# Performance work log

Hardware: AMD Instinct MI355X
Metric: run time of the kernel (lower is better)

Reference implementation:

```python
import jax, jax.numpy as jnp
import numpy as np
from math import factorial

# (mul, l, parity) for in1 == in2 == out
IRREPS = [(32, 0, 1), (32, 1, -1), (32, 2, 1)]
FEAT_DIM = sum(m * (2 * l + 1) for m, l, _ in IRREPS)  # 288
BATCH = 8192


def _cg(j1, m1, j2, m2, j3, m3):
    # Clebsch-Gordan <j1 m1 j2 m2 | j3 m3> (Racah formula), complex SH basis
    if m1 + m2 != m3 or not (abs(j1 - j2) <= j3 <= j1 + j2):
        return 0.0
    f = factorial
    pre = (2 * j3 + 1) * f(j3 + j1 - j2) * f(j3 - j1 + j2) * f(j1 + j2 - j3) / f(j1 + j2 + j3 + 1)
    pre *= f(j3 + m3) * f(j3 - m3) * f(j1 - m1) * f(j1 + m1) * f(j2 - m2) * f(j2 + m2)
    s = 0.0
    for k in range(0, j1 + j2 - j3 + 1):
        a = [k, j1 + j2 - j3 - k, j1 - m1 - k, j2 + m2 - k, j3 - j2 + m1 + k, j3 - j1 - m2 + k]
        if min(a) < 0:
            continue
        s += (-1.0) ** k / (f(a[0]) * f(a[1]) * f(a[2]) * f(a[3]) * f(a[4]) * f(a[5]))
    return np.sqrt(pre) * s


def _q(l):
    # unitary change of basis: real SH coords = Q @ complex SH coords
    Q = np.zeros((2 * l + 1, 2 * l + 1), dtype=np.complex128)
    Q[l, l] = 1.0
    for m in range(1, l + 1):
        Q[l + m, l + m] = (-1.0) ** m / np.sqrt(2.0)
        Q[l + m, l - m] = 1.0 / np.sqrt(2.0)
        Q[l - m, l - m] = 1j / np.sqrt(2.0)
        Q[l - m, l + m] = -1j * (-1.0) ** m / np.sqrt(2.0)
    return Q


def _wigner3j(l1, l2, l3):
    # real-basis Wigner 3j tensor, unit Frobenius norm (e3nn convention up to sign)
    C = np.zeros((2 * l1 + 1, 2 * l2 + 1, 2 * l3 + 1), dtype=np.complex128)
    for m1 in range(-l1, l1 + 1):
        for m2 in range(-l2, l2 + 1):
            m3 = -(m1 + m2)
            if abs(m3) <= l3:
                C[m1 + l1, m2 + l2, m3 + l3] = (-1.0) ** (l1 - l2 - m3) * _cg(l1, m1, l2, m2, l3, -m3)
    T = np.einsum('mnp,am,bn,cp->abc', C, _q(l1).conj(), _q(l2).conj(), _q(l3).conj())
    T = T.real if np.abs(T.real).sum() >= np.abs(T.imag).sum() else T.imag
    return (T / np.linalg.norm(T)).astype(np.float32)


def _instructions():
    # all parity- and triangle-allowed fully-connected 'uvw' paths
    ins = []
    for i1, (m1, l1, p1) in enumerate(IRREPS):
        for i2, (m2, l2, p2) in enumerate(IRREPS):
            for io, (mo, lo, po) in enumerate(IRREPS):
                if p1 * p2 == po and abs(l1 - l2) <= lo <= l1 + l2:
                    ins.append((i1, i2, io))
    return ins


N_WEIGHT = sum(IRREPS[i1][0] * IRREPS[i2][0] * IRREPS[io][0] for i1, i2, io in _instructions())  # 360448


def setup_inputs() -> dict:
    key = jax.random.key(0)
    k1, k2, k3 = jax.random.split(key, 3)
    return {
        'x1': jax.random.normal(k1, (BATCH, FEAT_DIM), jnp.float32),
        'x2': jax.random.normal(k2, (BATCH, FEAT_DIM), jnp.float32),
        'weight': jax.random.normal(k3, (N_WEIGHT,), jnp.float32),
    }


def _tp(x1, x2, weight):
    ins = _instructions()
    fan = {}
    for i1, i2, io in ins:  # 'element' path normalization fan-in per output irrep
        fan[io] = fan.get(io, 0) + IRREPS[i1][0] * IRREPS[i2][0]
    offs, o = [], 0
    for m, l, _ in IRREPS:
        offs.append(o)
        o += m * (2 * l + 1)
    z = x1.shape[0]
    out = [jnp.zeros((z, m * (2 * l + 1)), x1.dtype) for m, l, _ in IRREPS]
    w_off = 0
    for i1, i2, io in ins:
        m1, l1, _ = IRREPS[i1]
        m2, l2, _ = IRREPS[i2]
        mo, lo, _ = IRREPS[io]
        x1p = x1[:, offs[i1]:offs[i1] + m1 * (2 * l1 + 1)].reshape(z, m1, 2 * l1 + 1)
        x2p = x2[:, offs[i2]:offs[i2] + m2 * (2 * l2 + 1)].reshape(z, m2, 2 * l2 + 1)
        nw = m1 * m2 * mo
        W = weight[w_off:w_off + nw].reshape(m1, m2, mo)
        w_off += nw
        w3 = jnp.asarray(_wigner3j(l1, l2, lo))
        alpha = float(np.sqrt((2 * lo + 1) / fan[io]))  # component norm * 1/sqrt(fan_in)
        # contraction order chosen to keep intermediates small:
        t = jnp.einsum('zui,uvw->zivw', x1p, W)             # [z, 2l1+1, m2, mo]
        y = jnp.einsum('zivw,zvj,ijk->zwk', t, x2p, w3, optimize='optimal')
        out[io] = out[io] + alpha * y.reshape(z, -1)
    return jnp.concatenate(out, axis=1)


def reference(x1, x2, weight):
    return _tp(x1, x2, weight)
```

## Files before the change

### kernel.cpp

```cpp
#include <hip/hip_runtime.h>


__device__ float g_w3[11 * 128];


__device__ __forceinline__ double dfact(int n) {
    double r = 1.0;
    for (int i = 2; i <= n; ++i) r *= (double)i;
    return r;
}

__device__ double cg_coef(int j1, int m1, int j2, int m2, int j3, int m3) {
    if (m1 + m2 != m3) return 0.0;
    int lo = (j1 > j2) ? (j1 - j2) : (j2 - j1);
    if (j3 > j1 + j2 || j3 < lo) return 0.0;
    double pre = (2.0 * j3 + 1.0) * dfact(j3 + j1 - j2) * dfact(j3 - j1 + j2) *
                 dfact(j1 + j2 - j3) / dfact(j1 + j2 + j3 + 1);
    pre *= dfact(j3 + m3) * dfact(j3 - m3) * dfact(j1 - m1) * dfact(j1 + m1) *
           dfact(j2 - m2) * dfact(j2 + m2);
    double s = 0.0;
    for (int k = 0; k <= j1 + j2 - j3; ++k) {
        int a1 = j1 + j2 - j3 - k, a2 = j1 - m1 - k, a3 = j2 + m2 - k;
        int a4 = j3 - j2 + m1 + k, a5 = j3 - j1 - m2 + k;
        if (a1 < 0 || a2 < 0 || a3 < 0 || a4 < 0 || a5 < 0) continue;
        double t = 1.0 / (dfact(k) * dfact(a1) * dfact(a2) * dfact(a3) * dfact(a4) * dfact(a5));
        s += (k & 1) ? -t : t;
    }
    return sqrt(pre) * s;
}

__device__ __forceinline__ void qval(int l, int a, int mi, double& re, double& im) {
    re = 0.0; im = 0.0;
    const double inv = 0.7071067811865475244;
    int ma = a - l, mc = mi - l;
    if (ma == 0) { if (mc == 0) re = 1.0; return; }
    if (ma > 0) {
        if (mc == ma)        re = (ma & 1) ? -inv : inv;
        else if (mc == -ma)  re = inv;
    } else {
        int mm = -ma;
        if (mc == ma)        im = inv;
        else if (mc == -ma)  im = -((mm & 1) ? -inv : inv);
    }
}

__global__ void wigner3j_setup() {
    const int L1[11] = {0,0,0,1,1,1,1,2,2,2,2};
    const int L2[11] = {0,1,2,0,1,1,2,0,1,2,2};
    const int L3[11] = {0,1,2,1,0,2,1,2,1,0,2};
    const int p = blockIdx.x;
    const int l1 = L1[p], l2 = L2[p], l3 = L3[p];
    const int d1 = 2 * l1 + 1, d2 = 2 * l2 + 1, d3 = 2 * l3 + 1;
    const int n = d1 * d2 * d3;

    __shared__ double sre[125], sim[125];
    __shared__ double s_scale;
    __shared__ int s_im;

    const int e = threadIdx.x;
    if (e < n) {
        int a = e / (d2 * d3);
        int r = e - a * d2 * d3;
        int b = r / d3;
        int c = r - b * d3;
        double tre = 0.0, tim = 0.0;
        for (int m1 = -l1; m1 <= l1; ++m1) {
            for (int m2 = -l2; m2 <= l2; ++m2) {
                int m3 = -(m1 + m2);
                if (m3 < -l3 || m3 > l3) continue;
                int ex = l1 - l2 - m3;
                double sgn = (ex % 2 != 0) ? -1.0 : 1.0;
                double C = sgn * cg_coef(l1, m1, l2, m2, l3, -m3);
                if (C == 0.0) continue;
                double r1, i1, r2, i2, r3, i3;
                qval(l1, a, m1 + l1, r1, i1);
                qval(l2, b, m2 + l2, r2, i2);
                qval(l3, c, m3 + l3, r3, i3);
                i1 = -i1; i2 = -i2; i3 = -i3;
                double rr = r1 * r2 - i1 * i2;
                double ri = r1 * i2 + i1 * r2;
                double fr = rr * r3 - ri * i3;
                double fi = rr * i3 + ri * r3;
                tre += C * fr;
                tim += C * fi;
            }
        }
        sre[e] = tre; sim[e] = tim;
    }
    __syncthreads();
    if (threadIdx.x == 0) {
        double sar = 0.0, sai = 0.0;
        for (int i = 0; i < n; ++i) { sar += fabs(sre[i]); sai += fabs(sim[i]); }
        int useim = (sar >= sai) ? 0 : 1;
        double ss = 0.0;
        for (int i = 0; i < n; ++i) { double v = useim ? sim[i] : sre[i]; ss += v * v; }
        s_scale = 1.0 / sqrt(ss);
        s_im = useim;
    }
    __syncthreads();
    if (e < n) {
        double v = s_im ? sim[e] : sre[e];
        g_w3[p * 128 + e] = (float)(v * s_scale);
    }
}


__device__ __forceinline__ float f4c(const float4& v, int c) {
    switch (c & 3) {
        case 0:  return v.x;
        case 1:  return v.y;
        case 2:  return v.z;
        default: return v.w;
    }
}

template <int DH, int DS, int D1, int D2, int DO, bool HX1, int NW>
__device__ __forceinline__ void do_path(const float* __restrict__ xh,
                                        const float* __restrict__ xs,
                                        const float* __restrict__ Wp,
                                        const float* __restrict__ w3p,
                                        int k, float* __restrict__ acc) {
    float w3l[DH][DS];
#pragma unroll
    for (int ih = 0; ih < DH; ++ih) {
#pragma unroll
        for (int is = 0; is < DS; ++is) {
            const int i = HX1 ? ih : is;
            const int j = HX1 ? is : ih;
            w3l[ih][is] = w3p[(i * D2 + j) * DO + k];
        }
    }
    constexpr int CH = (DH >= 5) ? 16 : 32;
    static_assert((CH * DH) % 4 == 0, "H chunk must be float4-tileable");
#pragma unroll 1
    for (int h0 = 0; h0 < 32; h0 += CH) {
        float H[CH * DH];
#pragma unroll
        for (int q = 0; q < CH * DH / 4; ++q) {
            const float4 v = *reinterpret_cast<const float4*>(xh + h0 * DH + q * 4);
            H[q * 4 + 0] = v.x; H[q * 4 + 1] = v.y;
            H[q * 4 + 2] = v.z; H[q * 4 + 3] = v.w;
        }
#pragma unroll 2
        for (int g = 0; g < 8; ++g) {
            float4 bg[DS];
#pragma unroll
            for (int q = 0; q < DS; ++q)
                bg[q] = *reinterpret_cast<const float4*>(xs + g * 4 * DS + q * 4);
#pragma unroll
            for (int t = 0; t < 4; ++t) {
                const int s = g * 4 + t;
                float c[DH];
#pragma unroll
                for (int i = 0; i < DH; ++i) {
                    float cv = 0.f;
#pragma unroll
                    for (int j = 0; j < DS; ++j) {
                        const int e = t * DS + j;
                        cv = fmaf(w3l[i][j], f4c(bg[e >> 2], e), cv);
                    }
                    c[i] = cv;
                }
                const float* wbase = Wp + (HX1 ? s * 32 : s * 1024);
#pragma unroll
                for (int h = 0; h < CH; ++h) {
                    float o = 0.f;
#pragma unroll
                    for (int i = 0; i < DH; ++i) o = fmaf(c[i], H[h * DH + i], o);
                    const float* wr = wbase + (HX1 ? (h0 + h) * 1024 : (h0 + h) * 32);
#pragma unroll
                    for (int w = 0; w < NW; ++w) acc[w] = fmaf(wr[w], o, acc[w]);
                }
            }
        }
    }
}

__global__ __launch_bounds__(64, 2) void tp_main(const float* __restrict__ x1,
                                                 const float* __restrict__ x2,
                                                 const float* __restrict__ W,
                                                 float* __restrict__ out) {
    const int z = blockIdx.x * 64 + threadIdx.x;
    const float* r1 = x1 + (size_t)z * 288;
    const float* r2 = x2 + (size_t)z * 288;
    const int w0 = blockIdx.z * 16;
    const float* w3t = g_w3;

    float acc[16];
#pragma unroll
    for (int i = 0; i < 16; ++i) acc[i] = 0.f;

    const int arm = blockIdx.y;
    int io, k;
    if (arm == 0)      { io = 0; k = 0; }
    else if (arm <= 3) { io = 1; k = arm - 1; }
    else               { io = 2; k = arm - 4; }

    if (io == 0) {
        do_path<1, 1, 1, 1, 1, false, 16>(r2 + 0,   r1 + 0,   W + 0 * 32768 + w0,  w3t + 0 * 128, 0, acc);
        do_path<3, 3, 3, 3, 1, false, 16>(r2 + 32,  r1 + 32,  W + 4 * 32768 + w0,  w3t + 4 * 128, 0, acc);
        do_path<5, 5, 5, 5, 1, false, 16>(r2 + 128, r1 + 128, W + 9 * 32768 + w0,  w3t + 9 * 128, 0, acc);
    } else if (io == 1) {
        do_path<1, 3, 1, 3, 3, true,  16>(r1 + 0,   r2 + 32,  W + 1 * 32768 + w0,  w3t + 1 * 128, k, acc);
        do_path<1, 3, 3, 1, 3, false, 16>(r2 + 0,   r1 + 32,  W + 3 * 32768 + w0,  w3t + 3 * 128, k, acc);
        do_path<3, 5, 3, 5, 3, true,  16>(r1 + 32,  r2 + 128, W + 6 * 32768 + w0,  w3t + 6 * 128, k, acc);
        do_path<3, 5, 5, 3, 3, false, 16>(r2 + 32,  r1 + 128, W + 8 * 32768 + w0,  w3t + 8 * 128, k, acc);
    } else {
        do_path<1, 5, 1, 5, 5, true,  16>(r1 + 0,   r2 + 128, W + 2 * 32768 + w0,  w3t + 2 * 128, k, acc);
        do_path<3, 3, 3, 3, 5, false, 16>(r2 + 32,  r1 + 32,  W + 5 * 32768 + w0,  w3t + 5 * 128, k, acc);
        do_path<1, 5, 5, 1, 5, false, 16>(r2 + 0,   r1 + 128, W + 7 * 32768 + w0,  w3t + 7 * 128, k, acc);
        do_path<5, 5, 5, 5, 5, false, 16>(r2 + 128, r1 + 128, W + 10 * 32768 + w0, w3t + 10 * 128, k, acc);
    }

    const float alpha = (io == 0) ? 0.018042196f : ((io == 1) ? 0.027063294f : 0.034938562f);
    const int off_o   = (io == 0) ? 0 : ((io == 1) ? 32 : 128);
    const int DOd     = (io == 0) ? 1 : ((io == 1) ? 3 : 5);
    float* orow = out + (size_t)z * 288 + off_o + k;
#pragma unroll
    for (int w = 0; w < 16; ++w) orow[(w0 + w) * DOd] = alpha * acc[w];
}


extern "C" void kernel_launch(void* const* d_in, const int* in_sizes, int n_in,
                              void* d_out, int out_size, void* d_ws, size_t ws_size,
                              hipStream_t stream) {
    const float* x1 = (const float*)d_in[0];
    const float* x2 = (const float*)d_in[1];
    const float* W  = (const float*)d_in[2];
    float* out = (float*)d_out;

    wigner3j_setup<<<dim3(11), dim3(128), 0, stream>>>();
    tp_main<<<dim3(128, 9, 2), dim3(64), 0, stream>>>(x1, x2, W, out);
}
```

Before: 498.3 us.

## Stage per-path weight tiles into LDS with double-buffered async global loads

Weight rows used in the inner accumulation were read directly from global memory as wavefront-uniform loads. They are now copied into a two-slot LDS buffer with global_load_lds. The copy for the next slice is issued while the current slice is consumed, using manual vmcnt waits. The inner loop reads the 16 weights per h as four float4 LDS broadcasts. This aims to hide global or scalar-cache latency, but it costs 16 KB of LDS per 64-thread block, which may limit occupancy. It also relies on hand-written waitcnt values being correct alongside the other vector loads in flight.

```diff
diff --git a/kernel.cpp b/kernel.cpp
--- a/kernel.cpp
+++ b/kernel.cpp
@@ -114,12 +114,30 @@
     }
 }
 
-template <int DH, int DS, int D1, int D2, int DO, bool HX1, int NW>
+template <bool HX1, int CH>
+__device__ __forceinline__ void stage(const float* __restrict__ Wp,
+                                      float* buf, int s0, int h0, int lane) {
+#pragma unroll
+    for (int q = 0; q < 8; ++q) {
+        const int r = q * 16 + (lane >> 2);
+        const int seg = lane & 3;
+        const int s = s0 + ((CH == 16) ? (r >> 4) : (r >> 5));
+        const int h = h0 + ((CH == 16) ? (r & 15) : (r & 31));
+        const float* g = Wp + (HX1 ? h * 1024 + s * 32 : s * 1024 + h * 32) + seg * 4;
+        __builtin_amdgcn_global_load_lds(
+            (const __attribute__((address_space(1))) unsigned int*)g,
+            (__attribute__((address_space(3))) unsigned int*)(buf + q * 256),
+            16, 0, 0);
+    }
+}
+
+template <int DH, int DS, int D2, int DO, bool HX1>
 __device__ __forceinline__ void do_path(const float* __restrict__ xh,
                                         const float* __restrict__ xs,
                                         const float* __restrict__ Wp,
                                         const float* __restrict__ w3p,
-                                        int k, float* __restrict__ acc) {
+                                        int k, float* __restrict__ acc,
+                                        float (&lds)[2][2048], int lane) {
     float w3l[DH][DS];
 #pragma unroll
     for (int ih = 0; ih < DH; ++ih) {
@@ -131,6 +149,8 @@
         }
     }
     constexpr int CH = (DH >= 5) ? 16 : 32;
+    constexpr int ST = (DH >= 5) ? 8 : 4;
+    constexpr int NT = 32 / ST;
     static_assert((CH * DH) % 4 == 0, "H chunk must be float4-tileable");
 #pragma unroll 1
     for (int h0 = 0; h0 < 32; h0 += CH) {
@@ -141,35 +161,64 @@
             H[q * 4 + 0] = v.x; H[q * 4 + 1] = v.y;
             H[q * 4 + 2] = v.z; H[q * 4 + 3] = v.w;
         }
-#pragma unroll 2
-        for (int g = 0; g < 8; ++g) {
-            float4 bg[DS];
-#pragma unroll
-            for (int q = 0; q < DS; ++q)
-                bg[q] = *reinterpret_cast<const float4*>(xs + g * 4 * DS + q * 4);
-#pragma unroll
-            for (int t = 0; t < 4; ++t) {
-                const int s = g * 4 + t;
-                float c[DH];
-#pragma unroll
-                for (int i = 0; i < DH; ++i) {
-                    float cv = 0.f;
-#pragma unroll
-                    for (int j = 0; j < DS; ++j) {
-                        const int e = t * DS + j;
-                        cv = fmaf(w3l[i][j], f4c(bg[e >> 2], e), cv);
+        stage<HX1, CH>(Wp, &lds[0][0], 0, h0, lane);
+#pragma unroll 1
+        for (int t = 0; t < NT; ++t) {
+            if (t + 1 < NT) {
+                stage<HX1, CH>(Wp, &lds[(t + 1) & 1][0], (t + 1) * ST, h0, lane);
+                asm volatile("s_waitcnt vmcnt(8)" ::: "memory");
+            } else {
+                asm volatile("s_waitcnt vmcnt(0)" ::: "memory");
+            }
+            const float* wbuf = &lds[t & 1][0];
+#pragma unroll
+            for (int g = 0; g < ST / 4; ++g) {
+                float4 bg[DS];
+#pragma unroll
+                for (int q = 0; q < DS; ++q)
+                    bg[q] = *reinterpret_cast<const float4*>(
+                        xs + (t * ST + g * 4) * DS + q * 4);
+#pragma unroll
+                for (int tt = 0; tt < 4; ++tt) {
+                    const int ss = g * 4 + tt;
+                    float c[DH];
+#pragma unroll
+                    for (int i = 0; i < DH; ++i) {
+                        float cv = 0.f;
+#pragma unroll
+                        for (int j = 0; j < DS; ++j) {
+                            const int e = tt * DS + j;
+                            cv = fmaf(w3l[i][j], f4c(bg[e >> 2], e), cv);
+                        }
+                        c[i] = cv;
                     }
-                    c[i] = cv;
-                }
-                const float* wbase = Wp + (HX1 ? s * 32 : s * 1024);
-#pragma unroll
-                for (int h = 0; h < CH; ++h) {
-                    float o = 0.f;
-#pragma unroll
-                    for (int i = 0; i < DH; ++i) o = fmaf(c[i], H[h * DH + i], o);
-                    const float* wr = wbase + (HX1 ? (h0 + h) * 1024 : (h0 + h) * 32);
-#pragma unroll
-                    for (int w = 0; w < NW; ++w) acc[w] = fmaf(wr[w], o, acc[w]);
+#pragma unroll
+                    for (int h = 0; h < CH; ++h) {
+                        float o = 0.f;
+#pragma unroll
+                        for (int i = 0; i < DH; ++i) o = fmaf(c[i], H[h * DH + i], o);
+                        const float* wr = wbuf + (ss * CH + h) * 16;
+                        const float4 wa = *reinterpret_cast<const float4*>(wr);
+                        const float4 wb = *reinterpret_cast<const float4*>(wr + 4);
+                        const float4 wc = *reinterpret_cast<const float4*>(wr + 8);
+                        const float4 wd = *reinterpret_cast<const float4*>(wr + 12);
+                        acc[0]  = fmaf(wa.x, o, acc[0]);
+                        acc[1]  = fmaf(wa.y, o, acc[1]);
+                        acc[2]  = fmaf(wa.z, o, acc[2]);
+                        acc[3]  = fmaf(wa.w, o, acc[3]);
+                        acc[4]  = fmaf(wb.x, o, acc[4]);
+                        acc[5]  = fmaf(wb.y, o, acc[5]);
+                        acc[6]  = fmaf(wb.z, o, acc[6]);
+                        acc[7]  = fmaf(wb.w, o, acc[7]);
+                        acc[8]  = fmaf(wc.x, o, acc[8]);
+                        acc[9]  = fmaf(wc.y, o, acc[9]);
+                        acc[10] = fmaf(wc.z, o, acc[10]);
+                        acc[11] = fmaf(wc.w, o, acc[11]);
+                        acc[12] = fmaf(wd.x, o, acc[12]);
+                        acc[13] = fmaf(wd.y, o, acc[13]);
+                        acc[14] = fmaf(wd.z, o, acc[14]);
+                        acc[15] = fmaf(wd.w, o, acc[15]);
+                    }
                 }
             }
         }
@@ -180,7 +229,9 @@
                                                  const float* __restrict__ x2,
                                                  const float* __restrict__ W,
                                                  float* __restrict__ out) {
-    const int z = blockIdx.x * 64 + threadIdx.x;
+    __shared__ float lds[2][2048];
+    const int lane = threadIdx.x;
+    const int z = blockIdx.x * 64 + lane;
     const float* r1 = x1 + (size_t)z * 288;
     const float* r2 = x2 + (size_t)z * 288;
     const int w0 = blockIdx.z * 16;
@@ -197,19 +248,19 @@
     else               { io = 2; k = arm - 4; }
 
     if (io == 0) {
-        do_path<1, 1, 1, 1, 1, false, 16>(r2 + 0,   r1 + 0,   W + 0 * 32768 + w0,  w3t + 0 * 128, 0, acc);
-        do_path<3, 3, 3, 3, 1, false, 16>(r2 + 32,  r1 + 32,  W + 4 * 32768 + w0,  w3t + 4 * 128, 0, acc);
-        do_path<5, 5, 5, 5, 1, false, 16>(r2 + 128, r1 + 128, W + 9 * 32768 + w0,  w3t + 9 * 128, 0, acc);
+        do_path<1, 1, 1, 1, false>(r2 + 0,   r1 + 0,   W + 0 * 32768 + w0,  w3t + 0 * 128, 0, acc, lds, lane);
+        do_path<3, 3, 3, 1, false>(r2 + 32,  r1 + 32,  W + 4 * 32768 + w0,  w3t + 4 * 128, 0, acc, lds, lane);
+        do_path<5, 5, 5, 1, false>(r2 + 128, r1 + 128, W + 9 * 32768 + w0,  w3t + 9 * 128, 0, acc, lds, lane);
     } else if (io == 1) {
-        do_path<1, 3, 1, 3, 3, true,  16>(r1 + 0,   r2 + 32,  W + 1 * 32768 + w0,  w3t + 1 * 128, k, acc);
-        do_path<1, 3, 3, 1, 3, false, 16>(r2 + 0,   r1 + 32,  W + 3 * 32768 + w0,  w3t + 3 * 128, k, acc);
-        do_path<3, 5, 3, 5, 3, true,  16>(r1 + 32,  r2 + 128, W + 6 * 32768 + w0,  w3t + 6 * 128, k, acc);
-        do_path<3, 5, 5, 3, 3, false, 16>(r2 + 32,  r1 + 128, W + 8 * 32768 + w0,  w3t + 8 * 128, k, acc);
+        do_path<1, 3, 3, 3, true >(r1 + 0,   r2 + 32,  W + 1 * 32768 + w0,  w3t + 1 * 128, k, acc, lds, lane);
+        do_path<1, 3, 1, 3, false>(r2 + 0,   r1 + 32,  W + 3 * 32768 + w0,  w3t + 3 * 128, k, acc, lds, lane);
+        do_path<3, 5, 5, 3, true >(r1 + 32,  r2 + 128, W + 6 * 32768 + w0,  w3t + 6 * 128, k, acc, lds, lane);
+        do_path<3, 5, 3, 3, false>(r2 + 32,  r1 + 128, W + 8 * 32768 + w0,  w3t + 8 * 128, k, acc, lds, lane);
     } else {
-        do_path<1, 5, 1, 5, 5, true,  16>(r1 + 0,   r2 + 128, W + 2 * 32768 + w0,  w3t + 2 * 128, k, acc);
-        do_path<3, 3, 3, 3, 5, false, 16>(r2 + 32,  r1 + 32,  W + 5 * 32768 + w0,  w3t + 5 * 128, k, acc);
-        do_path<1, 5, 5, 1, 5, false, 16>(r2 + 0,   r1 + 128, W + 7 * 32768 + w0,  w3t + 7 * 128, k, acc);
-        do_path<5, 5, 5, 5, 5, false, 16>(r2 + 128, r1 + 128, W + 10 * 32768 + w0, w3t + 10 * 128, k, acc);
+        do_path<1, 5, 5, 5, true >(r1 + 0,   r2 + 128, W + 2 * 32768 + w0,  w3t + 2 * 128, k, acc, lds, lane);
+        do_path<3, 3, 3, 5, false>(r2 + 32,  r1 + 32,  W + 5 * 32768 + w0,  w3t + 5 * 128, k, acc, lds, lane);
+        do_path<1, 5, 1, 5, false>(r2 + 0,   r1 + 128, W + 7 * 32768 + w0,  w3t + 7 * 128, k, acc, lds, lane);
+        do_path<5, 5, 5, 5, false>(r2 + 128, r1 + 128, W + 10 * 32768 + w0, w3t + 10 * 128, k, acc, lds, lane);
     }
 
     const float alpha = (io == 0) ? 0.018042196f : ((io == 1) ? 0.027063294f : 0.034938562f);
```

New measurement: 474.5 us. 4.8% less time.
